# Optimization experiments

Hardware: AMD Instinct MI355X
Metric: run time of the kernel (lower is better)

Reference implementation:

```python
import jax, jax.numpy as jnp
import numpy as np
import math

B, N, D, SEQ = 4, 1024, 512, 256
HID, DIST_D, N_NER, N_LAB = 150, 128, 3, 4
SPANS_PER_WORD = 0.5
ASPECT, OPINION = 1, 2
NUM_DIST_EMB = 512


def setup_inputs() -> dict:
    key = jax.random.key(0)
    ks = jax.random.split(key, 9)
    starts = jax.random.randint(ks[0], (B, N), 0, SEQ)
    widths = jax.random.randint(ks[1], (B, N), 0, 8)
    ends = jnp.clip(starts + widths, 0, SEQ - 1)
    spans = jnp.stack([starts, ends], axis=-1).astype(jnp.int32)  # [B,N,2]
    ner_scores = jax.random.normal(ks[2], (B, N, N_NER), jnp.float32)
    span_embeddings = jax.random.normal(ks[3], (B, N, D), jnp.float32)
    span_mask = jnp.ones((B, N), dtype=bool)

    pair_dim = 2 * D + DIST_D

    def xavier(k, shape):
        std = math.sqrt(2.0 / (shape[0] + shape[1]))
        return jax.random.normal(k, shape, jnp.float32) * std

    dist_table = xavier(ks[4], (NUM_DIST_EMB, DIST_D))
    W1 = xavier(ks[5], (pair_dim, HID)); b1 = jnp.zeros((HID,), jnp.float32)
    W2 = xavier(ks[6], (HID, HID));      b2 = jnp.zeros((HID,), jnp.float32)
    Wc = xavier(ks[7], (HID, N_LAB));    bc = jnp.zeros((N_LAB,), jnp.float32)

    return dict(spans=spans, ner_scores=ner_scores, span_embeddings=span_embeddings,
                span_mask=span_mask, seq_length=SEQ, dist_table=dist_table,
                W1=W1, b1=b1, W2=W2, b2=b2, Wc=Wc, bc=bc)


def bucket_values(d, num_identity=4, num_total=10):
    # semi-logscale buckets: [0,1,2,3,4,5-7,8-15,16-31,32-63,64+]
    logspace = jnp.floor(jnp.log2(jnp.maximum(d, 1).astype(jnp.float32))).astype(jnp.int32) + (num_identity - 1)
    return jnp.clip(jnp.where(d <= num_identity, d, logspace), 0, num_total - 1)


def _prune(scores, mask, k):
    masked = jnp.where(mask, scores, jnp.float32(-1e20))
    _, idx = jax.lax.top_k(masked, k)  # [B,k]
    return idx


def reference(spans, ner_scores, span_embeddings, span_mask, seq_length,
              dist_table, W1, b1, W2, b2, Wc, bc):
    bsz, n_spans, d = span_embeddings.shape
    k = min(int(math.ceil(seq_length * SPANS_PER_WORD)), n_spans)

    a_idx = _prune(ner_scores[..., ASPECT], span_mask, k)    # [B,k]
    o_idx = _prune(ner_scores[..., OPINION], span_mask, k)
    a_keep = jnp.ones((bsz, k), dtype=bool)  # uniform seq_length -> all kept
    o_keep = a_keep

    gather = lambda t, i: jnp.take_along_axis(t, i[..., None], axis=1)
    a_emb = gather(span_embeddings, a_idx)   # [B,k,D]
    o_emb = gather(span_embeddings, o_idx)   # [B,k,D]
    spans_a = gather(spans, a_idx)           # [B,k,2]
    spans_o = gather(spans, o_idx)           # [B,k,2]

    # pairwise min span distance -> bucket -> embedding
    dis1 = jnp.abs(spans_a[..., 0][:, :, None] - spans_o[..., 1][:, None, :])
    dis2 = jnp.abs(spans_a[..., 1][:, :, None] - spans_o[..., 0][:, None, :])
    dis = jnp.minimum(dis1, dis2)                      # [B,k,k]
    dist_emb = dist_table[bucket_values(dis)]          # [B,k,k,DIST_D]

    pair = jnp.concatenate([
        jnp.broadcast_to(a_emb[:, :, None, :], (bsz, k, k, d)),
        jnp.broadcast_to(o_emb[:, None, :, :], (bsz, k, k, d)),
        dist_emb,
    ], axis=-1)                                        # [B,k,k,2D+DIST_D]

    # FeedForward (2 layers, ReLU, dropout=identity at eval) + classifier
    h = jax.nn.relu(pair @ W1 + b1)
    h = jax.nn.relu(h @ W2 + b2)
    scores = h @ Wc + bc                               # [B,k,k,n_labels]

    rel_mask = a_keep[:, :, None] & o_keep[:, None, :]
    return (jax.nn.softmax(scores, axis=-1), rel_mask, pair, spans_a, spans_o)
```

## Files before the change

kernel.cpp:

```cpp
#include <hip/hip_runtime.h>
#include <hip/hip_bf16.h>

#define BB 4
#define NN 1024
#define DD 512
#define KK 128
#define HID 150
#define HIDP 160
#define HSTRIDE 168
#define DIST_D 128
#define PAIRD 1152

typedef __attribute__((ext_vector_type(4))) float f32x4;
typedef __attribute__((ext_vector_type(8))) short s16x8;

__global__ __launch_bounds__(1024) void k_topk(const int* __restrict__ spans,
                                               const float* __restrict__ ner,
                                               int* ws_aidx, int* ws_oidx,
                                               int* ws_sa, int* ws_so,
                                               float* out3, float* out4) {
    __shared__ unsigned long long sk[NN];
    int t = threadIdx.x;
    int b = blockIdx.x >> 1;
    int which = blockIdx.x & 1;
    int ch = which ? 2 : 1;
    float v = ner[(b * NN + t) * 3 + ch];
    unsigned int u = __float_as_uint(v);
    unsigned int s = (u & 0x80000000u) ? ~u : (u ^ 0x80000000u);
    sk[t] = ((unsigned long long)s << 32) | (unsigned int)(NN - 1 - t);
    for (int ksz = 2; ksz <= NN; ksz <<= 1) {
        for (int jsz = ksz >> 1; jsz > 0; jsz >>= 1) {
            __syncthreads();
            int ixj = t ^ jsz;
            if (ixj > t) {
                unsigned long long k1 = sk[t], k2 = sk[ixj];
                bool before = k1 > k2;
                bool desc = ((t & ksz) == 0);
                if (desc ? !before : before) { sk[t] = k2; sk[ixj] = k1; }
            }
        }
    }
    __syncthreads();
    if (t < KK) {
        int idx = NN - 1 - (int)(unsigned int)(sk[t] & 0xffffffffu);
        int s0 = spans[(b * NN + idx) * 2];
        int s1 = spans[(b * NN + idx) * 2 + 1];
        int row = b * KK + t;
        if (which == 0) {
            ws_aidx[row] = idx;
            ws_sa[row * 2] = s0; ws_sa[row * 2 + 1] = s1;
            out3[row * 2] = (float)s0; out3[row * 2 + 1] = (float)s1;
        } else {
            ws_oidx[row] = idx;
            ws_so[row * 2] = s0; ws_so[row * 2 + 1] = s1;
            out4[row * 2] = (float)s0; out4[row * 2 + 1] = (float)s1;
        }
    }
}

__global__ __launch_bounds__(256) void k_contrib(const float* __restrict__ emb,
                                                 const float* __restrict__ dist_table,
                                                 const float* __restrict__ W1,
                                                 const float* __restrict__ b1,
                                                 const float* __restrict__ W2,
                                                 const int* __restrict__ ws_aidx,
                                                 const int* __restrict__ ws_oidx,
                                                 float* ws_ca, float* ws_co, float* ws_cd,
                                                 __hip_bfloat16* ws_w2t) {
    int bx = blockIdx.x, t = threadIdx.x;
    if (bx < 1024) {
        __shared__ float es[DD];
        int which = bx >> 9;
        int row = bx & 511;
        int b = row >> 7;
        int idx = which ? ws_oidx[row] : ws_aidx[row];
        const float* src = emb + ((size_t)(b * NN) + idx) * DD;
        for (int d = t; d < DD; d += 256) es[d] = src[d];
        __syncthreads();
        if (t < HIDP) {
            float acc = 0.f;
            if (t < HID) {
                const float* w = W1 + (size_t)(which * DD) * HID + t;
                float a0 = 0.f, a1 = 0.f, a2 = 0.f, a3 = 0.f;
                for (int d = 0; d < DD; d += 4) {
                    a0 = fmaf(es[d + 0], w[(size_t)(d + 0) * HID], a0);
                    a1 = fmaf(es[d + 1], w[(size_t)(d + 1) * HID], a1);
                    a2 = fmaf(es[d + 2], w[(size_t)(d + 2) * HID], a2);
                    a3 = fmaf(es[d + 3], w[(size_t)(d + 3) * HID], a3);
                }
                acc = (a0 + a1) + (a2 + a3);
            }
            (which ? ws_co : ws_ca)[row * HIDP + t] = acc;
        }
    } else if (bx < 1034) {
        int bk = bx - 1024;
        if (t < HIDP) {
            float acc = 0.f;
            if (t < HID) {
                acc = b1[t];
                for (int d = 0; d < DIST_D; ++d)
                    acc = fmaf(dist_table[bk * DIST_D + d], W1[(size_t)(2 * DD + d) * HID + t], acc);
            }
            ws_cd[bk * HIDP + t] = acc;
        }
    } else {
        int e = (bx - 1034) * 256 + t;
        if (e < HIDP * HSTRIDE) {
            int n = e / HSTRIDE, d = e - n * HSTRIDE;
            float v = (n < HID && d < HID) ? W2[d * HID + n] : 0.f;
            ws_w2t[e] = __float2bfloat16(v);
        }
    }
}

__global__ __launch_bounds__(256) void k_pair(const float* __restrict__ emb,
                                              const float* __restrict__ dist_table,
                                              const int* __restrict__ ws_aidx,
                                              const int* __restrict__ ws_oidx,
                                              const int* __restrict__ ws_sa,
                                              const int* __restrict__ ws_so,
                                              float* __restrict__ out1,
                                              float* __restrict__ out2) {
    __shared__ __align__(16) float a_s[DD];
    __shared__ __align__(16) float o_s[16 * DD];
    __shared__ __align__(16) float d_s[10 * DIST_D];
    __shared__ int bkt_s[16];
    __shared__ int oidx_s[16];

    int t = threadIdx.x;
    int blk = blockIdx.x;
    int bi = blk >> 3, jc = blk & 7;
    int b = bi >> 7;
    int j0 = jc << 4;

    int sa0 = ws_sa[bi * 2], sa1 = ws_sa[bi * 2 + 1];
    if (t < 16) {
        int j = j0 + t;
        oidx_s[t] = ws_oidx[b * KK + j];
        int so0 = ws_so[(b * KK + j) * 2], so1 = ws_so[(b * KK + j) * 2 + 1];
        int dd = min(abs(sa0 - so1), abs(sa1 - so0));
        bkt_s[t] = (dd <= 4) ? dd : min(34 - __clz(dd), 9);
        out1[bi * KK + j] = 1.0f;
    }
    __syncthreads();

    int aidx = ws_aidx[bi];
    const float4* asrc = (const float4*)(emb + ((size_t)(b * NN) + aidx) * DD);
    if (t < 128) ((float4*)a_s)[t] = asrc[t];
    for (int x = t; x < 320; x += 256)
        ((float4*)d_s)[x] = ((const float4*)dist_table)[x];
#pragma unroll
    for (int it = 0; it < 8; ++it) {
        int x = it * 256 + t;
        int j = x >> 7, c = x & 127;
        ((float4*)o_s)[x] = ((const float4*)(emb + ((size_t)(b * NN) + oidx_s[j]) * DD))[c];
    }
    __syncthreads();

    float4* dst = (float4*)(out2 + (size_t)bi * (KK * PAIRD)) + (size_t)j0 * 288;
#pragma unroll 6
    for (int it = 0; it < 18; ++it) {
        int f = it * 256 + t;
        int j = f / 288;
        int s = f - j * 288;
        float4 v;
        if (s < 128)      v = ((float4*)a_s)[s];
        else if (s < 256) v = ((float4*)o_s)[j * 128 + (s - 128)];
        else              v = ((float4*)d_s)[bkt_s[j] * 32 + (s - 256)];
        dst[f] = v;
    }
}

__global__ __launch_bounds__(256) void k_score(const float* __restrict__ Wc,
                                               const float* __restrict__ bcp,
                                               const float* __restrict__ b2p,
                                               const int* __restrict__ ws_sa,
                                               const int* __restrict__ ws_so,
                                               const float* __restrict__ ws_ca,
                                               const float* __restrict__ ws_co,
                                               const float* __restrict__ ws_cd,
                                               const __hip_bfloat16* __restrict__ ws_w2t,
                                               float* __restrict__ out0) {
    __shared__ float ca_s[HIDP];
    __shared__ float wc_s[HID * 4];
    __shared__ float b2_s[HIDP];
    __shared__ float bc_s[4];
    __shared__ int bkt_s[KK];
    __shared__ __align__(16) __hip_bfloat16 h1_s[KK * HSTRIDE];

    int t = threadIdx.x;
    int bi = blockIdx.x;
    int b = bi >> 7;

    if (t < HIDP) ca_s[t] = ws_ca[bi * HIDP + t];
    int sa0 = ws_sa[bi * 2], sa1 = ws_sa[bi * 2 + 1];
    if (t < KK) {
        int so0 = ws_so[(b * KK + t) * 2], so1 = ws_so[(b * KK + t) * 2 + 1];
        int dd = min(abs(sa0 - so1), abs(sa1 - so0));
        bkt_s[t] = (dd <= 4) ? dd : min(34 - __clz(dd), 9);
    }
    for (int x = t; x < HID * 4; x += 256) wc_s[x] = Wc[x];
    if (t < HIDP) b2_s[t] = (t < HID) ? b2p[t] : 0.f;
    if (t < 4) bc_s[t] = bcp[t];
    __syncthreads();

    for (int x = t; x < KK * HIDP; x += 256) {
        int j = x / HIDP, n = x - j * HIDP;
        float v = ca_s[n] + ws_co[(size_t)(b * KK + j) * HIDP + n] + ws_cd[bkt_s[j] * HIDP + n];
        h1_s[j * HSTRIDE + n] = __float2bfloat16(fmaxf(v, 0.f));
    }
    __syncthreads();

    int wave = t >> 6, l = t & 63;
    int lc = l & 15, lg = l >> 4;
    f32x4 acc[2][10];
#pragma unroll
    for (int mi = 0; mi < 2; ++mi)
#pragma unroll
        for (int nt = 0; nt < 10; ++nt)
            acc[mi][nt] = (f32x4){0.f, 0.f, 0.f, 0.f};

#pragma unroll
    for (int kk = 0; kk < 5; ++kk) {
        s16x8 af0 = *(const s16x8*)&h1_s[(wave * 32 + lc) * HSTRIDE + kk * 32 + lg * 8];
        s16x8 af1 = *(const s16x8*)&h1_s[(wave * 32 + 16 + lc) * HSTRIDE + kk * 32 + lg * 8];
#pragma unroll
        for (int nt = 0; nt < 10; ++nt) {
            s16x8 bf = *(const s16x8*)&ws_w2t[(nt * 16 + lc) * HSTRIDE + kk * 32 + lg * 8];
            acc[0][nt] = __builtin_amdgcn_mfma_f32_16x16x32_bf16(af0, bf, acc[0][nt], 0, 0, 0);
            acc[1][nt] = __builtin_amdgcn_mfma_f32_16x16x32_bf16(af1, bf, acc[1][nt], 0, 0, 0);
        }
    }

#pragma unroll
    for (int mi = 0; mi < 2; ++mi) {
#pragma unroll
        for (int r = 0; r < 4; ++r) {
            int j = wave * 32 + mi * 16 + lg * 4 + r;
            float p0 = 0.f, p1 = 0.f, p2 = 0.f, p3 = 0.f;
#pragma unroll
            for (int nt = 0; nt < 10; ++nt) {
                int n = nt * 16 + lc;
                if (n < HID) {
                    float h2 = fmaxf(acc[mi][nt][r] + b2_s[n], 0.f);
                    p0 = fmaf(h2, wc_s[n * 4 + 0], p0);
                    p1 = fmaf(h2, wc_s[n * 4 + 1], p1);
                    p2 = fmaf(h2, wc_s[n * 4 + 2], p2);
                    p3 = fmaf(h2, wc_s[n * 4 + 3], p3);
                }
            }
#pragma unroll
            for (int m = 8; m >= 1; m >>= 1) {
                p0 += __shfl_xor(p0, m, 16);
                p1 += __shfl_xor(p1, m, 16);
                p2 += __shfl_xor(p2, m, 16);
                p3 += __shfl_xor(p3, m, 16);
            }
            p0 += bc_s[0]; p1 += bc_s[1]; p2 += bc_s[2]; p3 += bc_s[3];
            float mx = fmaxf(fmaxf(p0, p1), fmaxf(p2, p3));
            float e0 = expf(p0 - mx), e1 = expf(p1 - mx), e2 = expf(p2 - mx), e3 = expf(p3 - mx);
            float inv = 1.f / (e0 + e1 + e2 + e3);
            if (lc < 4) {
                float v = (lc == 0) ? e0 : (lc == 1) ? e1 : (lc == 2) ? e2 : e3;
                out0[((size_t)bi * KK + j) * 4 + lc] = v * inv;
            }
        }
    }
}

extern "C" void kernel_launch(void* const* d_in, const int* in_sizes, int n_in,
                              void* d_out, int out_size, void* d_ws, size_t ws_size,
                              hipStream_t stream) {
    const int*   spans = (const int*)d_in[0];
    const float* ner   = (const float*)d_in[1];
    const float* emb   = (const float*)d_in[2];
    const float* dist_table = (const float*)d_in[5];
    const float* W1 = (const float*)d_in[6];
    const float* b1 = (const float*)d_in[7];
    const float* W2 = (const float*)d_in[8];
    const float* b2 = (const float*)d_in[9];
    const float* Wc = (const float*)d_in[10];
    const float* bc = (const float*)d_in[11];

    float* out0 = (float*)d_out;
    float* out1 = out0 + (size_t)BB * KK * KK * 4;
    float* out2 = out1 + (size_t)BB * KK * KK;
    float* out3 = out2 + (size_t)BB * KK * KK * PAIRD;
    float* out4 = out3 + (size_t)BB * KK * 2;

    int* ws_aidx = (int*)d_ws;
    int* ws_oidx = ws_aidx + BB * KK;
    int* ws_sa   = ws_oidx + BB * KK;
    int* ws_so   = ws_sa + BB * KK * 2;
    float* ws_ca = (float*)(ws_so + BB * KK * 2);
    float* ws_co = ws_ca + BB * KK * HIDP;
    float* ws_cd = ws_co + BB * KK * HIDP;
    __hip_bfloat16* ws_w2t = (__hip_bfloat16*)(ws_cd + 16 * HIDP);

    k_topk<<<8, 1024, 0, stream>>>(spans, ner, ws_aidx, ws_oidx, ws_sa, ws_so, out3, out4);
    k_contrib<<<1139, 256, 0, stream>>>(emb, dist_table, W1, b1, W2,
                                        ws_aidx, ws_oidx, ws_ca, ws_co, ws_cd, ws_w2t);
    k_pair<<<BB * KK * 8, 256, 0, stream>>>(emb, dist_table, ws_aidx, ws_oidx, ws_sa, ws_so,
                                            out1, out2);
    k_score<<<BB * KK, 256, 0, stream>>>(Wc, bc, b2, ws_sa, ws_so,
                                         ws_ca, ws_co, ws_cd, ws_w2t, out0);
}
```

Before: 114.6 us.

## Replace bitonic top-k with rank counting and fuse pair-write with scoring kernel

Top-k now ranks each element by counting larger keys instead of running a bitonic sort, and the dist-bucket and W2-transpose preparation move into that same launch. The embedding projection processes four rows per block so each W1 load is reused across rows. The pair-output writer and the MLP scoring kernel are merged into one interleaved grid, so the memory-bound output writes overlap the MFMA work and one launch is removed. The pair writer now reads opinion embeddings straight from global memory instead of staging them in shared memory. The costs are a 1024-element scan per thread for ranking and a large shared-memory footprint in the fused kernel, which may limit occupancy for the write-only blocks.

```diff
diff --git a/kernel.cpp b/kernel.cpp
--- a/kernel.cpp
+++ b/kernel.cpp
@@ -16,84 +16,47 @@
 
 __global__ __launch_bounds__(1024) void k_topk(const int* __restrict__ spans,
                                                const float* __restrict__ ner,
+                                               const float* __restrict__ dist_table,
+                                               const float* __restrict__ W1,
+                                               const float* __restrict__ b1,
+                                               const float* __restrict__ W2,
                                                int* ws_aidx, int* ws_oidx,
                                                int* ws_sa, int* ws_so,
+                                               float* ws_cd, __hip_bfloat16* ws_w2t,
                                                float* out3, float* out4) {
-    __shared__ unsigned long long sk[NN];
     int t = threadIdx.x;
-    int b = blockIdx.x >> 1;
-    int which = blockIdx.x & 1;
-    int ch = which ? 2 : 1;
-    float v = ner[(b * NN + t) * 3 + ch];
-    unsigned int u = __float_as_uint(v);
-    unsigned int s = (u & 0x80000000u) ? ~u : (u ^ 0x80000000u);
-    sk[t] = ((unsigned long long)s << 32) | (unsigned int)(NN - 1 - t);
-    for (int ksz = 2; ksz <= NN; ksz <<= 1) {
-        for (int jsz = ksz >> 1; jsz > 0; jsz >>= 1) {
-            __syncthreads();
-            int ixj = t ^ jsz;
-            if (ixj > t) {
-                unsigned long long k1 = sk[t], k2 = sk[ixj];
-                bool before = k1 > k2;
-                bool desc = ((t & ksz) == 0);
-                if (desc ? !before : before) { sk[t] = k2; sk[ixj] = k1; }
-            }
-        }
-    }
-    __syncthreads();
-    if (t < KK) {
-        int idx = NN - 1 - (int)(unsigned int)(sk[t] & 0xffffffffu);
-        int s0 = spans[(b * NN + idx) * 2];
-        int s1 = spans[(b * NN + idx) * 2 + 1];
-        int row = b * KK + t;
-        if (which == 0) {
-            ws_aidx[row] = idx;
-            ws_sa[row * 2] = s0; ws_sa[row * 2 + 1] = s1;
-            out3[row * 2] = (float)s0; out3[row * 2 + 1] = (float)s1;
-        } else {
-            ws_oidx[row] = idx;
-            ws_so[row * 2] = s0; ws_so[row * 2 + 1] = s1;
-            out4[row * 2] = (float)s0; out4[row * 2 + 1] = (float)s1;
-        }
-    }
-}
-
-__global__ __launch_bounds__(256) void k_contrib(const float* __restrict__ emb,
-                                                 const float* __restrict__ dist_table,
-                                                 const float* __restrict__ W1,
-                                                 const float* __restrict__ b1,
-                                                 const float* __restrict__ W2,
-                                                 const int* __restrict__ ws_aidx,
-                                                 const int* __restrict__ ws_oidx,
-                                                 float* ws_ca, float* ws_co, float* ws_cd,
-                                                 __hip_bfloat16* ws_w2t) {
-    int bx = blockIdx.x, t = threadIdx.x;
-    if (bx < 1024) {
-        __shared__ float es[DD];
-        int which = bx >> 9;
-        int row = bx & 511;
-        int b = row >> 7;
-        int idx = which ? ws_oidx[row] : ws_aidx[row];
-        const float* src = emb + ((size_t)(b * NN) + idx) * DD;
-        for (int d = t; d < DD; d += 256) es[d] = src[d];
+    int bx = blockIdx.x;
+    if (bx < 8) {
+        __shared__ unsigned long long sk[NN];
+        int b = bx >> 1;
+        int which = bx & 1;
+        int ch = which ? 2 : 1;
+        float v = ner[(b * NN + t) * 3 + ch];
+        unsigned int u = __float_as_uint(v);
+        unsigned int s = (u & 0x80000000u) ? ~u : (u ^ 0x80000000u);
+        unsigned long long mine = ((unsigned long long)s << 32) | (unsigned int)(NN - 1 - t);
+        sk[t] = mine;
         __syncthreads();
-        if (t < HIDP) {
-            float acc = 0.f;
-            if (t < HID) {
-                const float* w = W1 + (size_t)(which * DD) * HID + t;
-                float a0 = 0.f, a1 = 0.f, a2 = 0.f, a3 = 0.f;
-                for (int d = 0; d < DD; d += 4) {
-                    a0 = fmaf(es[d + 0], w[(size_t)(d + 0) * HID], a0);
-                    a1 = fmaf(es[d + 1], w[(size_t)(d + 1) * HID], a1);
-                    a2 = fmaf(es[d + 2], w[(size_t)(d + 2) * HID], a2);
-                    a3 = fmaf(es[d + 3], w[(size_t)(d + 3) * HID], a3);
-                }
-                acc = (a0 + a1) + (a2 + a3);
-            }
-            (which ? ws_co : ws_ca)[row * HIDP + t] = acc;
-        }
-    } else if (bx < 1034) {
-        int bk = bx - 1024;
+        int cnt = 0;
+#pragma unroll 16
+        for (int d = 0; d < NN; ++d) cnt += (sk[d] > mine) ? 1 : 0;
+        if (cnt < KK) {
+            int idx = t;
+            int s0 = spans[(b * NN + idx) * 2];
+            int s1 = spans[(b * NN + idx) * 2 + 1];
+            int row = b * KK + cnt;
+            if (which == 0) {
+                ws_aidx[row] = idx;
+                ws_sa[row * 2] = s0; ws_sa[row * 2 + 1] = s1;
+                out3[row * 2] = (float)s0; out3[row * 2 + 1] = (float)s1;
+            } else {
+                ws_oidx[row] = idx;
+                ws_so[row * 2] = s0; ws_so[row * 2 + 1] = s1;
+                out4[row * 2] = (float)s0; out4[row * 2 + 1] = (float)s1;
+            }
+        }
+    } else if (bx < 18) {
+        int bk = bx - 8;
         if (t < HIDP) {
             float acc = 0.f;
             if (t < HID) {
@@ -104,7 +67,7 @@
             ws_cd[bk * HIDP + t] = acc;
         }
     } else {
-        int e = (bx - 1034) * 256 + t;
+        int e = (bx - 18) * 1024 + t;
         if (e < HIDP * HSTRIDE) {
             int n = e / HSTRIDE, d = e - n * HSTRIDE;
             float v = (n < HID && d < HID) ? W2[d * HID + n] : 0.f;
@@ -113,157 +76,195 @@
     }
 }
 
-__global__ __launch_bounds__(256) void k_pair(const float* __restrict__ emb,
-                                              const float* __restrict__ dist_table,
-                                              const int* __restrict__ ws_aidx,
-                                              const int* __restrict__ ws_oidx,
-                                              const int* __restrict__ ws_sa,
-                                              const int* __restrict__ ws_so,
-                                              float* __restrict__ out1,
-                                              float* __restrict__ out2) {
-    __shared__ __align__(16) float a_s[DD];
-    __shared__ __align__(16) float o_s[16 * DD];
-    __shared__ __align__(16) float d_s[10 * DIST_D];
-    __shared__ int bkt_s[16];
-    __shared__ int oidx_s[16];
-
+__global__ __launch_bounds__(256) void k_contrib(const float* __restrict__ emb,
+                                                 const float* __restrict__ W1,
+                                                 const int* __restrict__ ws_aidx,
+                                                 const int* __restrict__ ws_oidx,
+                                                 float* ws_ca, float* ws_co) {
+    __shared__ __align__(16) float es[4][DD];
     int t = threadIdx.x;
-    int blk = blockIdx.x;
-    int bi = blk >> 3, jc = blk & 7;
-    int b = bi >> 7;
-    int j0 = jc << 4;
-
-    int sa0 = ws_sa[bi * 2], sa1 = ws_sa[bi * 2 + 1];
-    if (t < 16) {
-        int j = j0 + t;
-        oidx_s[t] = ws_oidx[b * KK + j];
-        int so0 = ws_so[(b * KK + j) * 2], so1 = ws_so[(b * KK + j) * 2 + 1];
-        int dd = min(abs(sa0 - so1), abs(sa1 - so0));
-        bkt_s[t] = (dd <= 4) ? dd : min(34 - __clz(dd), 9);
-        out1[bi * KK + j] = 1.0f;
+    int bx = blockIdx.x;
+    int which = bx >> 7;
+    int row0 = (bx & 127) * 4;
+    const int* idxsrc = which ? ws_oidx : ws_aidx;
+    for (int x = t; x < 512; x += 256) {
+        int r = x >> 7, c = x & 127;
+        int row = row0 + r;
+        int b = row >> 7;
+        int idx = idxsrc[row];
+        ((float4*)es[r])[c] = ((const float4*)(emb + ((size_t)(b * NN) + idx) * DD))[c];
     }
     __syncthreads();
-
-    int aidx = ws_aidx[bi];
-    const float4* asrc = (const float4*)(emb + ((size_t)(b * NN) + aidx) * DD);
-    if (t < 128) ((float4*)a_s)[t] = asrc[t];
-    for (int x = t; x < 320; x += 256)
-        ((float4*)d_s)[x] = ((const float4*)dist_table)[x];
-#pragma unroll
-    for (int it = 0; it < 8; ++it) {
-        int x = it * 256 + t;
-        int j = x >> 7, c = x & 127;
-        ((float4*)o_s)[x] = ((const float4*)(emb + ((size_t)(b * NN) + oidx_s[j]) * DD))[c];
-    }
-    __syncthreads();
-
-    float4* dst = (float4*)(out2 + (size_t)bi * (KK * PAIRD)) + (size_t)j0 * 288;
-#pragma unroll 6
-    for (int it = 0; it < 18; ++it) {
-        int f = it * 256 + t;
-        int j = f / 288;
-        int s = f - j * 288;
-        float4 v;
-        if (s < 128)      v = ((float4*)a_s)[s];
-        else if (s < 256) v = ((float4*)o_s)[j * 128 + (s - 128)];
-        else              v = ((float4*)d_s)[bkt_s[j] * 32 + (s - 256)];
-        dst[f] = v;
+    if (t < HIDP) {
+        float a0 = 0.f, a1 = 0.f, a2 = 0.f, a3 = 0.f;
+        if (t < HID) {
+            const float* w = W1 + (size_t)(which * DD) * HID + t;
+#pragma unroll 4
+            for (int d4 = 0; d4 < 128; ++d4) {
+                float4 e0 = ((const float4*)es[0])[d4];
+                float4 e1 = ((const float4*)es[1])[d4];
+                float4 e2 = ((const float4*)es[2])[d4];
+                float4 e3 = ((const float4*)es[3])[d4];
+                float w0 = w[(size_t)(4 * d4 + 0) * HID];
+                float w1v = w[(size_t)(4 * d4 + 1) * HID];
+                float w2v = w[(size_t)(4 * d4 + 2) * HID];
+                float w3 = w[(size_t)(4 * d4 + 3) * HID];
+                a0 = fmaf(e0.x, w0, a0); a0 = fmaf(e0.y, w1v, a0); a0 = fmaf(e0.z, w2v, a0); a0 = fmaf(e0.w, w3, a0);
+                a1 = fmaf(e1.x, w0, a1); a1 = fmaf(e1.y, w1v, a1); a1 = fmaf(e1.z, w2v, a1); a1 = fmaf(e1.w, w3, a1);
+                a2 = fmaf(e2.x, w0, a2); a2 = fmaf(e2.y, w1v, a2); a2 = fmaf(e2.z, w2v, a2); a2 = fmaf(e2.w, w3, a2);
+                a3 = fmaf(e3.x, w0, a3); a3 = fmaf(e3.y, w1v, a3); a3 = fmaf(e3.z, w2v, a3); a3 = fmaf(e3.w, w3, a3);
+            }
+        }
+        float* dstb = which ? ws_co : ws_ca;
+        dstb[(row0 + 0) * HIDP + t] = a0;
+        dstb[(row0 + 1) * HIDP + t] = a1;
+        dstb[(row0 + 2) * HIDP + t] = a2;
+        dstb[(row0 + 3) * HIDP + t] = a3;
     }
 }
 
-__global__ __launch_bounds__(256) void k_score(const float* __restrict__ Wc,
+__global__ __launch_bounds__(256) void k_fused(const float* __restrict__ emb,
+                                               const float* __restrict__ dist_table,
+                                               const float* __restrict__ Wc,
                                                const float* __restrict__ bcp,
                                                const float* __restrict__ b2p,
+                                               const int* __restrict__ ws_aidx,
+                                               const int* __restrict__ ws_oidx,
                                                const int* __restrict__ ws_sa,
                                                const int* __restrict__ ws_so,
                                                const float* __restrict__ ws_ca,
                                                const float* __restrict__ ws_co,
                                                const float* __restrict__ ws_cd,
                                                const __hip_bfloat16* __restrict__ ws_w2t,
-                                               float* __restrict__ out0) {
-    __shared__ float ca_s[HIDP];
-    __shared__ float wc_s[HID * 4];
-    __shared__ float b2_s[HIDP];
-    __shared__ float bc_s[4];
-    __shared__ int bkt_s[KK];
-    __shared__ __align__(16) __hip_bfloat16 h1_s[KK * HSTRIDE];
-
+                                               float* __restrict__ out0,
+                                               float* __restrict__ out1,
+                                               float* __restrict__ out2) {
+    __shared__ __align__(16) char smem[47232];
     int t = threadIdx.x;
-    int bi = blockIdx.x;
-    int b = bi >> 7;
-
-    if (t < HIDP) ca_s[t] = ws_ca[bi * HIDP + t];
-    int sa0 = ws_sa[bi * 2], sa1 = ws_sa[bi * 2 + 1];
-    if (t < KK) {
-        int so0 = ws_so[(b * KK + t) * 2], so1 = ws_so[(b * KK + t) * 2 + 1];
-        int dd = min(abs(sa0 - so1), abs(sa1 - so0));
-        bkt_s[t] = (dd <= 4) ? dd : min(34 - __clz(dd), 9);
-    }
-    for (int x = t; x < HID * 4; x += 256) wc_s[x] = Wc[x];
-    if (t < HIDP) b2_s[t] = (t < HID) ? b2p[t] : 0.f;
-    if (t < 4) bc_s[t] = bcp[t];
-    __syncthreads();
-
-    for (int x = t; x < KK * HIDP; x += 256) {
-        int j = x / HIDP, n = x - j * HIDP;
-        float v = ca_s[n] + ws_co[(size_t)(b * KK + j) * HIDP + n] + ws_cd[bkt_s[j] * HIDP + n];
-        h1_s[j * HSTRIDE + n] = __float2bfloat16(fmaxf(v, 0.f));
-    }
-    __syncthreads();
-
-    int wave = t >> 6, l = t & 63;
-    int lc = l & 15, lg = l >> 4;
-    f32x4 acc[2][10];
-#pragma unroll
-    for (int mi = 0; mi < 2; ++mi)
-#pragma unroll
-        for (int nt = 0; nt < 10; ++nt)
-            acc[mi][nt] = (f32x4){0.f, 0.f, 0.f, 0.f};
-
-#pragma unroll
-    for (int kk = 0; kk < 5; ++kk) {
-        s16x8 af0 = *(const s16x8*)&h1_s[(wave * 32 + lc) * HSTRIDE + kk * 32 + lg * 8];
-        s16x8 af1 = *(const s16x8*)&h1_s[(wave * 32 + 16 + lc) * HSTRIDE + kk * 32 + lg * 8];
-#pragma unroll
-        for (int nt = 0; nt < 10; ++nt) {
-            s16x8 bf = *(const s16x8*)&ws_w2t[(nt * 16 + lc) * HSTRIDE + kk * 32 + lg * 8];
-            acc[0][nt] = __builtin_amdgcn_mfma_f32_16x16x32_bf16(af0, bf, acc[0][nt], 0, 0, 0);
-            acc[1][nt] = __builtin_amdgcn_mfma_f32_16x16x32_bf16(af1, bf, acc[1][nt], 0, 0, 0);
-        }
-    }
-
-#pragma unroll
-    for (int mi = 0; mi < 2; ++mi) {
-#pragma unroll
-        for (int r = 0; r < 4; ++r) {
-            int j = wave * 32 + mi * 16 + lg * 4 + r;
-            float p0 = 0.f, p1 = 0.f, p2 = 0.f, p3 = 0.f;
+    int bx = blockIdx.x;
+
+    if (bx % 9 == 0) {
+        int bi = bx / 9;
+        int b = bi >> 7;
+        __hip_bfloat16* h1_s = (__hip_bfloat16*)smem;
+        float* ca_s = (float*)(smem + 43008);
+        float* wc_s = (float*)(smem + 43648);
+        float* b2_s = (float*)(smem + 46048);
+        float* bc_s = (float*)(smem + 46688);
+        int* bkt_s  = (int*)(smem + 46704);
+
+        if (t < HIDP) ca_s[t] = ws_ca[bi * HIDP + t];
+        int sa0 = ws_sa[bi * 2], sa1 = ws_sa[bi * 2 + 1];
+        if (t < KK) {
+            int so0 = ws_so[(b * KK + t) * 2], so1 = ws_so[(b * KK + t) * 2 + 1];
+            int dd = min(abs(sa0 - so1), abs(sa1 - so0));
+            bkt_s[t] = (dd <= 4) ? dd : min(34 - __clz(dd), 9);
+        }
+        for (int x = t; x < HID * 4; x += 256) wc_s[x] = Wc[x];
+        if (t < HIDP) b2_s[t] = (t < HID) ? b2p[t] : 0.f;
+        if (t < 4) bc_s[t] = bcp[t];
+        __syncthreads();
+
+        for (int x = t; x < KK * HIDP; x += 256) {
+            int j = x / HIDP, n = x - j * HIDP;
+            float v = ca_s[n] + ws_co[(size_t)(b * KK + j) * HIDP + n] + ws_cd[bkt_s[j] * HIDP + n];
+            h1_s[j * HSTRIDE + n] = __float2bfloat16(fmaxf(v, 0.f));
+        }
+        __syncthreads();
+
+        int wave = t >> 6, l = t & 63;
+        int lc = l & 15, lg = l >> 4;
+        f32x4 acc[2][10];
+#pragma unroll
+        for (int mi = 0; mi < 2; ++mi)
+#pragma unroll
+            for (int nt = 0; nt < 10; ++nt)
+                acc[mi][nt] = (f32x4){0.f, 0.f, 0.f, 0.f};
+
+#pragma unroll
+        for (int kk = 0; kk < 5; ++kk) {
+            s16x8 af0 = *(const s16x8*)&h1_s[(wave * 32 + lc) * HSTRIDE + kk * 32 + lg * 8];
+            s16x8 af1 = *(const s16x8*)&h1_s[(wave * 32 + 16 + lc) * HSTRIDE + kk * 32 + lg * 8];
 #pragma unroll
             for (int nt = 0; nt < 10; ++nt) {
-                int n = nt * 16 + lc;
-                if (n < HID) {
-                    float h2 = fmaxf(acc[mi][nt][r] + b2_s[n], 0.f);
-                    p0 = fmaf(h2, wc_s[n * 4 + 0], p0);
-                    p1 = fmaf(h2, wc_s[n * 4 + 1], p1);
-                    p2 = fmaf(h2, wc_s[n * 4 + 2], p2);
-                    p3 = fmaf(h2, wc_s[n * 4 + 3], p3);
+                s16x8 bf = *(const s16x8*)&ws_w2t[(nt * 16 + lc) * HSTRIDE + kk * 32 + lg * 8];
+                acc[0][nt] = __builtin_amdgcn_mfma_f32_16x16x32_bf16(af0, bf, acc[0][nt], 0, 0, 0);
+                acc[1][nt] = __builtin_amdgcn_mfma_f32_16x16x32_bf16(af1, bf, acc[1][nt], 0, 0, 0);
+            }
+        }
+
+#pragma unroll
+        for (int mi = 0; mi < 2; ++mi) {
+#pragma unroll
+            for (int r = 0; r < 4; ++r) {
+                int j = wave * 32 + mi * 16 + lg * 4 + r;
+                float p0 = 0.f, p1 = 0.f, p2 = 0.f, p3 = 0.f;
+#pragma unroll
+                for (int nt = 0; nt < 10; ++nt) {
+                    int n = nt * 16 + lc;
+                    if (n < HID) {
+                        float h2 = fmaxf(acc[mi][nt][r] + b2_s[n], 0.f);
+                        p0 = fmaf(h2, wc_s[n * 4 + 0], p0);
+                        p1 = fmaf(h2, wc_s[n * 4 + 1], p1);
+                        p2 = fmaf(h2, wc_s[n * 4 + 2], p2);
+                        p3 = fmaf(h2, wc_s[n * 4 + 3], p3);
+                    }
                 }
-            }
-#pragma unroll
-            for (int m = 8; m >= 1; m >>= 1) {
-                p0 += __shfl_xor(p0, m, 16);
-                p1 += __shfl_xor(p1, m, 16);
-                p2 += __shfl_xor(p2, m, 16);
-                p3 += __shfl_xor(p3, m, 16);
-            }
-            p0 += bc_s[0]; p1 += bc_s[1]; p2 += bc_s[2]; p3 += bc_s[3];
-            float mx = fmaxf(fmaxf(p0, p1), fmaxf(p2, p3));
-            float e0 = expf(p0 - mx), e1 = expf(p1 - mx), e2 = expf(p2 - mx), e3 = expf(p3 - mx);
-            float inv = 1.f / (e0 + e1 + e2 + e3);
-            if (lc < 4) {
-                float v = (lc == 0) ? e0 : (lc == 1) ? e1 : (lc == 2) ? e2 : e3;
-                out0[((size_t)bi * KK + j) * 4 + lc] = v * inv;
-            }
+#pragma unroll
+                for (int m = 8; m >= 1; m >>= 1) {
+                    p0 += __shfl_xor(p0, m, 16);
+                    p1 += __shfl_xor(p1, m, 16);
+                    p2 += __shfl_xor(p2, m, 16);
+                    p3 += __shfl_xor(p3, m, 16);
+                }
+                p0 += bc_s[0]; p1 += bc_s[1]; p2 += bc_s[2]; p3 += bc_s[3];
+                float mx = fmaxf(fmaxf(p0, p1), fmaxf(p2, p3));
+                float e0 = expf(p0 - mx), e1 = expf(p1 - mx), e2 = expf(p2 - mx), e3 = expf(p3 - mx);
+                float inv = 1.f / (e0 + e1 + e2 + e3);
+                if (lc < 4) {
+                    float v = (lc == 0) ? e0 : (lc == 1) ? e1 : (lc == 2) ? e2 : e3;
+                    out0[((size_t)bi * KK + j) * 4 + lc] = v * inv;
+                }
+            }
+        }
+    } else {
+        int pid = bx - bx / 9 - 1;
+        int bi = pid >> 3, jc = pid & 7;
+        int b = bi >> 7;
+        int j0 = jc << 4;
+        float* a_s  = (float*)smem;
+        float* d_s  = (float*)(smem + 2048);
+        int* bkt_s  = (int*)(smem + 7168);
+        int* oidx_s = (int*)(smem + 7232);
+
+        int sa0 = ws_sa[bi * 2], sa1 = ws_sa[bi * 2 + 1];
+        if (t < 16) {
+            int j = j0 + t;
+            oidx_s[t] = ws_oidx[b * KK + j];
+            int so0 = ws_so[(b * KK + j) * 2], so1 = ws_so[(b * KK + j) * 2 + 1];
+            int dd = min(abs(sa0 - so1), abs(sa1 - so0));
+            bkt_s[t] = (dd <= 4) ? dd : min(34 - __clz(dd), 9);
+            out1[bi * KK + j] = 1.0f;
+        }
+        int aidx = ws_aidx[bi];
+        const float4* asrc = (const float4*)(emb + ((size_t)(b * NN) + aidx) * DD);
+        if (t < 128) ((float4*)a_s)[t] = asrc[t];
+        for (int x = t; x < 320; x += 256)
+            ((float4*)d_s)[x] = ((const float4*)dist_table)[x];
+        __syncthreads();
+
+        const float4* ebase = (const float4*)(emb + (size_t)b * NN * DD);
+        float4* dst = (float4*)(out2 + (size_t)bi * (KK * PAIRD)) + (size_t)j0 * 288;
+#pragma unroll 6
+        for (int it = 0; it < 18; ++it) {
+            int f = it * 256 + t;
+            int j = f / 288;
+            int s = f - j * 288;
+            float4 v;
+            if (s < 128)      v = ((float4*)a_s)[s];
+            else if (s < 256) v = ebase[(size_t)oidx_s[j] * 128 + (s - 128)];
+            else              v = ((float4*)d_s)[bkt_s[j] * 32 + (s - 256)];
+            dst[f] = v;
         }
     }
 }
@@ -297,11 +298,12 @@
     float* ws_cd = ws_co + BB * KK * HIDP;
     __hip_bfloat16* ws_w2t = (__hip_bfloat16*)(ws_cd + 16 * HIDP);
 
-    k_topk<<<8, 1024, 0, stream>>>(spans, ner, ws_aidx, ws_oidx, ws_sa, ws_so, out3, out4);
-    k_contrib<<<1139, 256, 0, stream>>>(emb, dist_table, W1, b1, W2,
-                                        ws_aidx, ws_oidx, ws_ca, ws_co, ws_cd, ws_w2t);
-    k_pair<<<BB * KK * 8, 256, 0, stream>>>(emb, dist_table, ws_aidx, ws_oidx, ws_sa, ws_so,
-                                            out1, out2);
-    k_score<<<BB * KK, 256, 0, stream>>>(Wc, bc, b2, ws_sa, ws_so,
-                                         ws_ca, ws_co, ws_cd, ws_w2t, out0);
+    k_topk<<<45, 1024, 0, stream>>>(spans, ner, dist_table, W1, b1, W2,
+                                    ws_aidx, ws_oidx, ws_sa, ws_so,
+                                    ws_cd, ws_w2t, out3, out4);
+    k_contrib<<<256, 256, 0, stream>>>(emb, W1, ws_aidx, ws_oidx, ws_ca, ws_co);
+    k_fused<<<9 * BB * KK, 256, 0, stream>>>(emb, dist_table, Wc, bc, b2,
+                                             ws_aidx, ws_oidx, ws_sa, ws_so,
+                                             ws_ca, ws_co, ws_cd, ws_w2t,
+                                             out0, out1, out2);
 }
```

Result: slower. 138.8 us (+21.1%).
